# Optimization experiments

Hardware: AMD Instinct MI355X
Metric: run time of the kernel (lower is better)

Reference implementation:

```python
import jax, jax.numpy as jnp
import numpy as np

D = 512; N_HEAD = 8; D_HEAD = 64; D_INNER = 2048; SEG = 512; N_LAYER = 2; BATCH = 32
NUM_ITEMS = 50000
OMEGA = [2, 3, 4, 5, 7, 11, 21, 50]  # len == N_HEAD, required by multi-scale mask broadcast
EPS = 1e-8
STD = 0.02


def _layer_norm(x, w, b):
    mu = x.mean(-1, keepdims=True)
    var = ((x - mu) ** 2).mean(-1, keepdims=True)
    return (x - mu) / jnp.sqrt(var + EPS) * w + b


def _masks():
    # dir_mask: triu(ones, 1) (reverse=False); ms_mask[i,j,m] per omega band
    dir_mask = jnp.triu(jnp.ones((SEG, SEG), jnp.float32), 1)
    ms = np.stack([np.tri(SEG, SEG, o - 1) != np.tri(SEG, SEG, -o) for o in OMEGA], axis=-1)
    return dir_mask, jnp.asarray(ms)


def _pos_emb():
    freq = jnp.arange(0, D, 2, dtype=jnp.float32)
    inv_freq = 1.0 / jnp.power(10000.0, freq / D)
    pos_seq = jnp.arange(SEG, -SEG, -1.0, dtype=jnp.float32)  # length 2*SEG
    sinusoid = pos_seq[:, None] * inv_freq[None, :]
    return jnp.concatenate([jnp.sin(sinusoid), jnp.cos(sinusoid)], axis=-1)  # (2S, D)


def _rel_shift_bnij(x, klen):
    b, n, i, j2 = x.shape
    x = x.reshape(b, n, j2, i)[:, :, 1:, :].reshape(b, n, i, j2 - 1)
    return x[:, :, :, :klen]


def setup_inputs() -> dict:
    key = jax.random.key(0)
    ks = jax.random.split(key, 16)
    L = N_LAYER
    item_emb = STD * jax.random.normal(ks[0], (NUM_ITEMS + 1, D), jnp.float32)
    item_emb = item_emb.at[0].set(0.0)  # padding_idx=0
    proj = lambda k: STD * jax.random.normal(k, (L, D, N_HEAD, D_HEAD), jnp.float32)
    return {
        "input_ids": jax.random.randint(ks[1], (BATCH, SEG), 0, NUM_ITEMS + 1),
        "input_mask": jnp.zeros((BATCH, SEG), jnp.float32),
        "item_emb": item_emb,
        "Wq": proj(ks[2]), "Wk": proj(ks[3]), "Wv": proj(ks[4]),
        "Wr": proj(ks[5]), "Wo": proj(ks[6]),
        "r_r_bias": STD * jax.random.normal(ks[7], (L, N_HEAD, D_HEAD), jnp.float32),
        "r_w_bias": STD * jax.random.normal(ks[8], (L, N_HEAD, D_HEAD), jnp.float32),
        "ln_attn_w": jnp.ones((L, D), jnp.float32), "ln_attn_b": jnp.zeros((L, D), jnp.float32),
        "W1": STD * jax.random.normal(ks[9], (L, D, D_INNER), jnp.float32),
        "b1": jnp.zeros((L, D_INNER), jnp.float32),
        "W2": STD * jax.random.normal(ks[10], (L, D_INNER, D), jnp.float32),
        "b2": jnp.zeros((L, D), jnp.float32),
        "ln_ff_w": jnp.ones((L, D), jnp.float32), "ln_ff_b": jnp.zeros((L, D), jnp.float32),
    }


def reference(input_ids, input_mask, item_emb, Wq, Wk, Wv, Wr, Wo, r_r_bias, r_w_bias,
              ln_attn_w, ln_attn_b, W1, b1, W2, b2, ln_ff_w, ln_ff_b):
    ids = input_ids.T                      # (S, B)
    im = input_mask.T.astype(jnp.float32)  # (S, B)
    dir_mask, ms_mask = _masks()
    # data_mask: (q,k,b); attn_mask: (q,k,b,n) via multi-scale bands (training path)
    data_mask = im[None, :, :] + im[:, None, :] + dir_mask[:, :, None]
    attn_mask = ((data_mask[:, :, :, None] + (~ms_mask)[:, :, None, :].astype(jnp.float32)) > 0).astype(jnp.float32)
    mask_bnij = jnp.transpose(attn_mask, (2, 3, 0, 1))  # (b,n,i,j)

    h = item_emb[ids]          # (S, B, D)
    pos = _pos_emb()           # (2S, D), shared across batch
    scale = 1.0 / np.sqrt(D_HEAD).astype(np.float32)

    for l in range(N_LAYER):
        k_h = jnp.einsum('ibh,hnd->ibnd', h, Wk[l])
        v_h = jnp.einsum('ibh,hnd->ibnd', h, Wv[l])
        k_r = jnp.einsum('jh,hnd->jnd', pos, Wr[l])   # pos shared across batch
        q_h = jnp.einsum('ibh,hnd->ibnd', h, Wq[l])
        ac = jnp.einsum('ibnd,jbnd->bnij', q_h + r_w_bias[l], k_h)
        bd = jnp.einsum('ibnd,jnd->bnij', q_h + r_r_bias[l], k_r)
        bd = _rel_shift_bnij(bd, SEG)
        attn_score = (ac + bd) * scale - 1e30 * mask_bnij
        attn_prob = jax.nn.softmax(attn_score, axis=3)
        attn_vec = jnp.einsum('bnij,jbnd->ibnd', attn_prob, v_h)
        attn_out = jnp.einsum('ibnd,hnd->ibh', attn_vec, Wo[l])
        h = _layer_norm(attn_out + h, ln_attn_w[l], ln_attn_b[l])
        ff = jax.nn.gelu(h @ W1[l] + b1[l], approximate=False) @ W2[l] + b2[l]
        h = _layer_norm(ff + h, ln_ff_w[l], ln_ff_b[l])

    return jnp.transpose(h, (1, 0, 2))  # (B, S, D)
```

## Files before the change

kernel.cpp:

```cpp
#include <hip/hip_runtime.h>
#include <math.h>


#define S_  512
#define B_  32
#define D_  512
#define NH  8
#define DH  64
#define DI  2048
#define M_  (S_*B_)
#define QKV_LD 1536
#define WL  3407872
#define FP32_ONE 0x3F800000u

typedef unsigned short ushort_t;
typedef __attribute__((ext_vector_type(8))) short short8;
typedef __attribute__((ext_vector_type(4))) float f32x4;

__constant__ int OMEGA_C[8] = {2, 3, 4, 5, 7, 11, 21, 50};

__device__ __forceinline__ float b2f(ushort_t us) {
    return __uint_as_float(((unsigned int)us) << 16);
}
__device__ __forceinline__ ushort_t f2b(float f) {
    unsigned int u = __float_as_uint(f);
    return (ushort_t)((u + 0x7fffu + ((u >> 16) & 1u)) >> 16);
}
__device__ __forceinline__ float ldx(const void* p, size_t idx, bool isbf) {
    return isbf ? b2f(((const ushort_t*)p)[idx]) : ((const float*)p)[idx];
}
__device__ __forceinline__ void async16(const ushort_t* g, ushort_t* l) {
    __builtin_amdgcn_global_load_lds(
        (const __attribute__((address_space(1))) unsigned int*)g,
        (__attribute__((address_space(3))) unsigned int*)l, 16, 0, 0);
}

#define DPPA(v, ctrl) v += __int_as_float(__builtin_amdgcn_update_dpp(0, __float_as_int(v), ctrl, 0xf, 0xf, true))
__device__ __forceinline__ void dpp_sum64(float& v) {
    DPPA(v, 0x111); DPPA(v, 0x112); DPPA(v, 0x114);
    DPPA(v, 0x118); DPPA(v, 0x142); DPPA(v, 0x143);
}
#define DPPROR(v, ctrl) __int_as_float(__builtin_amdgcn_update_dpp(__float_as_int(v), __float_as_int(v), ctrl, 0xf, 0xf, false))
__device__ __forceinline__ float row16_sum(float v) {
    v += DPPROR(v, 0x128); v += DPPROR(v, 0x124);
    v += DPPROR(v, 0x122); v += DPPROR(v, 0x121);
    return v;
}
__device__ __forceinline__ float row16_max(float v) {
    v = fmaxf(v, DPPROR(v, 0x128)); v = fmaxf(v, DPPROR(v, 0x124));
    v = fmaxf(v, DPPROR(v, 0x122)); v = fmaxf(v, DPPROR(v, 0x121));
    return v;
}

__global__ __launch_bounds__(256) void embed_kernel(const int* __restrict__ ids,
                                                    const void* __restrict__ emb,
                                                    ushort_t* __restrict__ h,
                                                    const unsigned int* __restrict__ dtp) {
    const bool isbf = (dtp[0] != FP32_ONE);
    int flat = blockIdx.x * 256 + threadIdx.x;
    int d = flat & (D_ - 1);
    int row = flat >> 9;
    int s = row >> 5, b = row & 31;
    int id = ids[b * S_ + s];
    size_t src = (size_t)id * D_ + d;
    h[flat] = isbf ? ((const ushort_t*)emb)[src] : f2b(((const float*)emb)[src]);
}

__global__ __launch_bounds__(256) void posemb_kernel(ushort_t* __restrict__ pos) {
    int flat = blockIdx.x * 256 + threadIdx.x;
    int p = flat >> 8, k = flat & 255;
    float inv = expf((float)k * -0.035977892078031f);
    float val = (512.0f - (float)p) * inv;
    pos[p * D_ + k]       = f2b(sinf(val));
    pos[p * D_ + 256 + k] = f2b(cosf(val));
}

__global__ __launch_bounds__(256) void transp_cvt4(
    const void* __restrict__ s0, const void* __restrict__ s1,
    const void* __restrict__ s2, const void* __restrict__ s3,
    ushort_t* __restrict__ wbuf, const unsigned int* __restrict__ dtp) {
    const bool isbf = (dtp[0] != FP32_ONE);
    __shared__ float tt[32][33];
    int z = blockIdx.z, layer = z >> 2, t4 = z & 3;
    const void* srcs[4] = {s0, s1, s2, s3};
    const void* in = srcs[t4];
    size_t inoff = (size_t)layer * 262144;
    ushort_t* out = wbuf + (size_t)layer * WL + (size_t)t4 * 262144;
    int tx = threadIdx.x & 31, ty = threadIdx.x >> 5;
    int n0 = blockIdx.x * 32, k0 = blockIdx.y * 32;
#pragma unroll
    for (int it = 0; it < 4; ++it)
        tt[ty + it * 8][tx] = ldx(in, inoff + (size_t)(k0 + ty + it * 8) * 512 + n0 + tx, isbf);
    __syncthreads();
#pragma unroll
    for (int it = 0; it < 4; ++it)
        out[(size_t)(n0 + ty + it * 8) * 512 + k0 + tx] = f2b(tt[tx][ty + it * 8]);
}

__global__ __launch_bounds__(256) void transp_cvtL(const void* __restrict__ in, size_t perlin,
                                                   ushort_t* __restrict__ wbuf, size_t outoff,
                                                   const unsigned int* __restrict__ dtp,
                                                   int K, int N) {
    const bool isbf = (dtp[0] != FP32_ONE);
    __shared__ float tt[32][33];
    int layer = blockIdx.z;
    size_t inoff = (size_t)layer * perlin;
    ushort_t* out = wbuf + (size_t)layer * WL + outoff;
    int tx = threadIdx.x & 31, ty = threadIdx.x >> 5;
    int n0 = blockIdx.x * 32, k0 = blockIdx.y * 32;
#pragma unroll
    for (int it = 0; it < 4; ++it)
        tt[ty + it * 8][tx] = ldx(in, inoff + (size_t)(k0 + ty + it * 8) * N + n0 + tx, isbf);
    __syncthreads();
#pragma unroll
    for (int it = 0; it < 4; ++it)
        out[(size_t)(n0 + ty + it * 8) * K + k0 + tx] = f2b(tt[tx][ty + it * 8]);
}

__global__ __launch_bounds__(256) void cvtL(const void* __restrict__ in, size_t perlin,
                                            ushort_t* __restrict__ wbuf, size_t outoff,
                                            const unsigned int* __restrict__ dtp, int nelem) {
    const bool isbf = (dtp[0] != FP32_ONE);
    int layer = blockIdx.z;
    int i = blockIdx.x * 256 + threadIdx.x;
    if (i < nelem)
        wbuf[(size_t)layer * WL + outoff + i] = f2b(ldx(in, (size_t)layer * perlin + i, isbf));
}

template<int EPI, int OUT>
__global__ __launch_bounds__(256)
void mfma_gemm(const ushort_t* __restrict__ A, int lda,
               const ushort_t* __restrict__ Bt, int ldb,
               const void* __restrict__ biasv, size_t biasoff,
               void* __restrict__ Cv, int ldc,
               const unsigned int* __restrict__ dtp, int M, int N, int K) {
    const bool isbf = (dtp[0] != FP32_ONE);
    __shared__ ushort_t As[128 * 32];
    __shared__ ushort_t Bs[128 * 32];
    const int tid = threadIdx.x;
    const int bm = blockIdx.x * 128, bn = blockIdx.y * 128;
    const int w = tid >> 6, lane = tid & 63;
    const int wr = w >> 1, wc = w & 1;
    const int quad = lane >> 4, l16 = lane & 15;
    const int rsub = lane >> 2;
    const int kcg  = (lane & 3) ^ ((rsub >> 1) & 3);
    const int fsw  = (l16 >> 1) & 3;

    f32x4 acc[4][4];
#pragma unroll
    for (int i = 0; i < 4; ++i)
#pragma unroll
        for (int j = 0; j < 4; ++j)
#pragma unroll
            for (int r = 0; r < 4; ++r) acc[i][j][r] = 0.f;

    for (int k0 = 0; k0 < K; k0 += 32) {
#pragma unroll
        for (int c = 0; c < 2; ++c) {
            int grp = c * 4 + w;
            int row = grp * 16 + rsub;
            async16(A  + (size_t)(bm + row) * lda + k0 + kcg * 8, As + grp * 512);
            async16(Bt + (size_t)(bn + row) * ldb + k0 + kcg * 8, Bs + grp * 512);
        }
        __syncthreads();

        short8 af[4], bf[4];
#pragma unroll
        for (int t = 0; t < 4; ++t) {
            int ra = wr * 64 + t * 16 + l16;
            int rb = wc * 64 + t * 16 + l16;
            af[t] = *(const short8*)(As + ra * 32 + ((quad ^ fsw) * 8));
            bf[t] = *(const short8*)(Bs + rb * 32 + ((quad ^ fsw) * 8));
        }
#pragma unroll
        for (int tr = 0; tr < 4; ++tr)
#pragma unroll
            for (int tc = 0; tc < 4; ++tc)
                acc[tr][tc] = __builtin_amdgcn_mfma_f32_16x16x32_bf16(af[tr], bf[tc], acc[tr][tc], 0, 0, 0);
        __syncthreads();
    }

#pragma unroll
    for (int tc = 0; tc < 4; ++tc) {
        int gcol = bn + wc * 64 + tc * 16 + l16;
        float bv = 0.f;
        if (EPI >= 1) bv = ldx(biasv, biasoff + gcol, isbf);
#pragma unroll
        for (int tr = 0; tr < 4; ++tr) {
            int rbase = bm + wr * 64 + tr * 16 + quad * 4;
#pragma unroll
            for (int r = 0; r < 4; ++r) {
                float x = acc[tr][tc][r] + bv;
                if (EPI == 2) x = 0.5f * x * (1.f + erff(x * 0.7071067811865475f));
                size_t coff = (size_t)(rbase + r) * ldc + gcol;
                if (OUT == 0)      ((ushort_t*)Cv)[coff] = f2b(x);
                else if (OUT == 1) ((float*)Cv)[coff] = x;
                else               ((float*)Cv)[coff] += x;
            }
        }
    }
}

__global__ __launch_bounds__(256) void attn_mfma(
    ushort_t* __restrict__ qkv, const ushort_t* __restrict__ krb,
    const void* __restrict__ rwb, const void* __restrict__ rrb, size_t boff,
    const void* __restrict__ im,
    const unsigned int* __restrict__ dtp) {
    const bool isbf = (dtp[0] != FP32_ONE);
    __shared__ ushort_t Ks[128 * 64];
    __shared__ ushort_t VT[64 * 128];
    __shared__ ushort_t Rs[64 * 64];
    __shared__ float    BD2[4 * 16 * 64];
    __shared__ ushort_t Ps[4 * 16 * 128];
    __shared__ float    imk[128];
    __shared__ float    imq[64];

    const int tid = threadIdx.x;
    const int i0 = blockIdx.x * 64;
    const int b  = blockIdx.y;
    const int n  = blockIdx.z;
    const int o  = OMEGA_C[n];
    const int noff = n * DH;
    const int j0 = i0 - 64;
    const int w = tid >> 6, lane = tid & 63;
    const int quad = lane >> 4, l16 = lane & 15;

#pragma unroll
    for (int it = 0; it < 4; ++it) {
        int q4 = it * 256 + tid;
        int c  = q4 >> 3, ch = q4 & 7;
        int jc = j0 + c; jc = jc < 0 ? 0 : jc;
        size_t rowb = (size_t)(jc * B_ + b) * QKV_LD + noff;
        *(uint4*)(Ks + c * 64 + ch * 8) = *(const uint4*)(qkv + rowb + 512 + ch * 8);
        ushort_t v8[8];
        *(uint4*)v8 = *(const uint4*)(qkv + rowb + 1024 + ch * 8);
#pragma unroll
        for (int e = 0; e < 8; ++e) VT[(ch * 8 + e) * 128 + c] = v8[e];
    }
#pragma unroll
    for (int it = 0; it < 2; ++it) {
        int q4 = it * 256 + tid;
        int m = q4 >> 3, ch = q4 & 7;
        *(uint4*)(Rs + m * 64 + ch * 8) =
            *(const uint4*)(krb + (size_t)(512 - m) * 512 + noff + ch * 8);
    }
    if (tid < 128) {
        int j = j0 + tid;
        imk[tid] = (j >= 0) ? ldx(im, b * S_ + j, isbf) : 0.f;
    } else if (tid < 192) {
        imq[tid - 128] = ldx(im, b * S_ + i0 + (tid - 128), isbf);
    }
    __syncthreads();

    const int qrow = i0 + w * 16 + l16;
    size_t qbase = (size_t)(qrow * B_ + b) * QKV_LD + noff;
    short8 aw[2], ar[2];
#pragma unroll
    for (int kc = 0; kc < 2; ++kc) {
        int kof = kc * 32 + quad * 8;
        ushort_t qe[8];
        *(uint4*)qe = *(const uint4*)(qkv + qbase + kof);
#pragma unroll
        for (int e = 0; e < 8; ++e) {
            float f = b2f(qe[e]);
            ((ushort_t*)&aw[kc])[e] = f2b(f + ldx(rwb, boff + noff + kof + e, isbf));
            ((ushort_t*)&ar[kc])[e] = f2b(f + ldx(rrb, boff + noff + kof + e, isbf));
        }
    }

    f32x4 accs[8];
#pragma unroll
    for (int ct = 0; ct < 8; ++ct) {
        short8 b0 = *(const short8*)(Ks + (ct * 16 + l16) * 64 + quad * 8);
        short8 b1 = *(const short8*)(Ks + (ct * 16 + l16) * 64 + 32 + quad * 8);
        f32x4 z = {0.f, 0.f, 0.f, 0.f};
        z = __builtin_amdgcn_mfma_f32_16x16x32_bf16(aw[0], b0, z, 0, 0, 0);
        z = __builtin_amdgcn_mfma_f32_16x16x32_bf16(aw[1], b1, z, 0, 0, 0);
        accs[ct] = z;
    }
    float* BD2w = BD2 + w * 16 * 64;
#pragma unroll
    for (int mt = 0; mt < 4; ++mt) {
        short8 b0 = *(const short8*)(Rs + (mt * 16 + l16) * 64 + quad * 8);
        short8 b1 = *(const short8*)(Rs + (mt * 16 + l16) * 64 + 32 + quad * 8);
        f32x4 z = {0.f, 0.f, 0.f, 0.f};
        z = __builtin_amdgcn_mfma_f32_16x16x32_bf16(ar[0], b0, z, 0, 0, 0);
        z = __builtin_amdgcn_mfma_f32_16x16x32_bf16(ar[1], b1, z, 0, 0, 0);
#pragma unroll
        for (int r = 0; r < 4; ++r)
            BD2w[(quad * 4 + r) * 64 + mt * 16 + l16] = z[r];
    }

    float im_i[4];
#pragma unroll
    for (int r = 0; r < 4; ++r) im_i[r] = imq[w * 16 + quad * 4 + r];

    float sc[8][4];
#pragma unroll
    for (int ct = 0; ct < 8; ++ct) {
        int cl = ct * 16 + l16;
        float imk_c = imk[cl];
#pragma unroll
        for (int r = 0; r < 4; ++r) {
            int qrl = w * 16 + quad * 4 + r;
            int rel = qrl + 64 - cl;
            int relc = rel < 0 ? 0 : (rel > 63 ? 63 : rel);
            float bd = BD2w[(quad * 4 + r) * 64 + relc];
            bool valid = (rel >= 0) && (rel < o) && (rel <= i0 + qrl)
                         && (im_i[r] + imk_c <= 0.f);
            sc[ct][r] = valid ? (accs[ct][r] + bd) * 0.125f : -1e30f;
        }
    }
    float rl[4];
#pragma unroll
    for (int r = 0; r < 4; ++r) {
        float mx = sc[0][r];
#pragma unroll
        for (int ct = 1; ct < 8; ++ct) mx = fmaxf(mx, sc[ct][r]);
        mx = row16_max(mx);
        float l = 0.f;
#pragma unroll
        for (int ct = 0; ct < 8; ++ct) {
            float pv = expf(sc[ct][r] - mx);
            sc[ct][r] = pv;
            l += pv;
        }
        l = row16_sum(l);
        rl[r] = 1.f / l;
    }
    ushort_t* Pw = Ps + w * 16 * 128;
#pragma unroll
    for (int ct = 0; ct < 8; ++ct)
#pragma unroll
        for (int r = 0; r < 4; ++r)
            Pw[(quad * 4 + r) * 128 + ct * 16 + l16] = f2b(sc[ct][r]);

    short8 aP[4];
#pragma unroll
    for (int kc = 0; kc < 4; ++kc)
        aP[kc] = *(const short8*)(Pw + l16 * 128 + kc * 32 + quad * 8);

#pragma unroll
    for (int dt = 0; dt < 4; ++dt) {
        f32x4 accO = {0.f, 0.f, 0.f, 0.f};
#pragma unroll
        for (int kc = 0; kc < 4; ++kc) {
            short8 bV = *(const short8*)(VT + (dt * 16 + l16) * 128 + kc * 32 + quad * 8);
            accO = __builtin_amdgcn_mfma_f32_16x16x32_bf16(aP[kc], bV, accO, 0, 0, 0);
        }
#pragma unroll
        for (int r = 0; r < 4; ++r) {
            int qg = i0 + w * 16 + quad * 4 + r;
            qkv[(size_t)(qg * B_ + b) * QKV_LD + noff + dt * 16 + l16] = f2b(accO[r] * rl[r]);
        }
    }
}

template<int XF>
__global__ __launch_bounds__(256) void add_ln_kernel(
    const void* __restrict__ x, ushort_t* __restrict__ h,
    const void* __restrict__ w, const void* __restrict__ b, size_t boff,
    const unsigned int* __restrict__ dtp) {
    const bool isbf = (dtp[0] != FP32_ONE);
    int row = blockIdx.x;
    size_t base = (size_t)row * D_;
    int tid = threadIdx.x;
    float x0 = XF ? ((const float*)x)[base + tid]       : b2f(((const ushort_t*)x)[base + tid]);
    float x1 = XF ? ((const float*)x)[base + 256 + tid] : b2f(((const ushort_t*)x)[base + 256 + tid]);
    float v0 = x0 + b2f(h[base + tid]);
    float v1 = x1 + b2f(h[base + 256 + tid]);
    float s = v0 + v1, ss = v0 * v0 + v1 * v1;
    dpp_sum64(s); dpp_sum64(ss);
    __shared__ float red[8];
    int wv = tid >> 6, lane = tid & 63;
    if (lane == 63) { red[wv] = s; red[4 + wv] = ss; }
    __syncthreads();
    float S  = red[0] + red[1] + red[2] + red[3];
    float SS = red[4] + red[5] + red[6] + red[7];
    float mu  = S * (1.f / D_);
    float var = fmaxf(SS * (1.f / D_) - mu * mu, 0.f);
    float inv = rsqrtf(var + 1e-8f);
    h[base + tid]       = f2b((v0 - mu) * inv * ldx(w, boff + tid, isbf)       + ldx(b, boff + tid, isbf));
    h[base + 256 + tid] = f2b((v1 - mu) * inv * ldx(w, boff + 256 + tid, isbf) + ldx(b, boff + 256 + tid, isbf));
}

__global__ __launch_bounds__(256) void writeout_kernel(const ushort_t* __restrict__ h,
                                                       void* __restrict__ out,
                                                       const unsigned int* __restrict__ dtp) {
    const bool isbf = (dtp[0] != FP32_ONE);
    int flat = blockIdx.x * 256 + threadIdx.x;
    int d = flat & (D_ - 1);
    int rest = flat >> 9;
    int s = rest & (S_ - 1), b = rest >> 9;
    ushort_t v = h[((size_t)(s * B_ + b) << 9) + d];
    if (isbf) ((ushort_t*)out)[flat] = v;
    else      ((float*)out)[flat] = b2f(v);
}

extern "C" void kernel_launch(void* const* d_in, const int* in_sizes, int n_in,
                              void* d_out, int out_size, void* d_ws, size_t ws_size,
                              hipStream_t stream) {
    (void)in_sizes; (void)n_in; (void)out_size; (void)ws_size;
    const int*  ids = (const int*)d_in[0];
    const void* im  = d_in[1];
    const void* emb = d_in[2];
    const void* Wq = d_in[3], *Wk = d_in[4], *Wv = d_in[5], *Wr = d_in[6], *Wo = d_in[7];
    const void* rrb = d_in[8], *rwb = d_in[9];
    const void* lnaw = d_in[10], *lnab = d_in[11];
    const void* W1 = d_in[12], *b1 = d_in[13], *W2 = d_in[14], *b2 = d_in[15];
    const void* lnfw = d_in[16], *lnfb = d_in[17];
    const unsigned int* dtp = (const unsigned int*)d_in[10];

    char* wsb = (char*)d_ws;
    ushort_t* h     = (ushort_t*)wsb;
    ushort_t* qkv   = (ushort_t*)(wsb + (16u << 20));
    ushort_t* ff1c  = (ushort_t*)(wsb + (16u << 20));
    float*    acc32 = (float*)   (wsb + (48u << 20));
    ushort_t* tmp   = (ushort_t*)(wsb + (64u << 20));
    ushort_t* wbuf  = (ushort_t*)(wsb + (80u << 20));
    ushort_t* posb  = (ushort_t*)(wsb + (93u << 20));
    ushort_t* krb   = (ushort_t*)(wsb + (94u << 20));

    embed_kernel<<<32768, 256, 0, stream>>>(ids, emb, h, dtp);
    posemb_kernel<<<1024, 256, 0, stream>>>(posb);

    transp_cvt4<<<dim3(16, 16, 8), 256, 0, stream>>>(Wq, Wk, Wv, Wr, wbuf, dtp);
    cvtL<<<dim3(1024, 1, 2), 256, 0, stream>>>(Wo, 262144, wbuf, 1048576, dtp, 262144);
    transp_cvtL<<<dim3(64, 16, 2), 256, 0, stream>>>(W1, 1048576, wbuf, 1310720, dtp, 512, 2048);
    transp_cvtL<<<dim3(16, 64, 2), 256, 0, stream>>>(W2, 1048576, wbuf, 2359296, dtp, 2048, 512);

    for (int l = 0; l < 2; ++l) {
        size_t boff = (size_t)l * 512;
        size_t b1off = (size_t)l * 2048;
        ushort_t* qkvT = wbuf + (size_t)l * WL;
        ushort_t* wrT  = qkvT + 786432;
        ushort_t* woc  = wrT  + 262144;
        ushort_t* w1T  = woc  + 262144;
        ushort_t* w2T  = w1T  + 1048576;

        mfma_gemm<0,0><<<dim3(8, 4), 256, 0, stream>>>(posb, 512, wrT, 512, nullptr, 0, krb, 512, dtp, 1024, 512, 512);
        mfma_gemm<0,0><<<dim3(128, 12), 256, 0, stream>>>(h, 512, qkvT, 512, nullptr, 0, qkv, QKV_LD, dtp, M_, QKV_LD, 512);

        attn_mfma<<<dim3(8, 32, 8), 256, 0, stream>>>(qkv, krb, rwb, rrb, boff, im, dtp);

        mfma_gemm<0,0><<<dim3(128, 4), 256, 0, stream>>>(qkv, QKV_LD, woc, 512, nullptr, 0, tmp, 512, dtp, M_, 512, 512);
        add_ln_kernel<0><<<16384, 256, 0, stream>>>(tmp, h, lnaw, lnab, boff, dtp);

        for (int nh = 0; nh < 2; ++nh) {
            ushort_t* w1part = w1T + (size_t)nh * 1024 * 512;
            ushort_t* w2part = w2T + (size_t)nh * 1024;
            mfma_gemm<2,0><<<dim3(128, 8), 256, 0, stream>>>(h, 512, w1part, 512, b1, b1off + nh * 1024, ff1c, 1024, dtp, M_, 1024, 512);
            if (nh == 0)
                mfma_gemm<1,1><<<dim3(128, 4), 256, 0, stream>>>(ff1c, 1024, w2part, 2048, b2, boff, acc32, 512, dtp, M_, 512, 1024);
            else
                mfma_gemm<0,2><<<dim3(128, 4), 256, 0, stream>>>(ff1c, 1024, w2part, 2048, nullptr, 0, acc32, 512, dtp, M_, 512, 1024);
        }
        add_ln_kernel<1><<<16384, 256, 0, stream>>>(acc32, h, lnfw, lnfb, boff, dtp);
    }

    writeout_kernel<<<32768, 256, 0, stream>>>(h, d_out, dtp);
}
```

Before: 842.8 us.

## Vectorize embed, layernorm, writeout and GEMM/attention epilogue stores

The embed, writeout and add+layernorm kernels now process 8 elements per thread with 128-bit loads and stores, and layernorm uses one wave per row with a readlane reduction instead of shared memory. The GEMM and attention epilogues swap the MFMA operand order so each lane holds contiguous output columns, which lets results be written as packed 64- or 128-bit stores instead of scattered 16-bit ones. Softmax normalization moves into the P write. The attention kernel still computes the old accO product but discards it, which adds redundant MFMA work unless the compiler eliminates it.

```diff
diff --git a/kernel.cpp b/kernel.cpp
--- a/kernel.cpp
+++ b/kernel.cpp
@@ -51,19 +51,33 @@
     v = fmaxf(v, DPPROR(v, 0x122)); v = fmaxf(v, DPPROR(v, 0x121));
     return v;
 }
+__device__ __forceinline__ float rlane(float v, int l) {
+    return __int_as_float(__builtin_amdgcn_readlane(__float_as_int(v), l));
+}
 
 __global__ __launch_bounds__(256) void embed_kernel(const int* __restrict__ ids,
                                                     const void* __restrict__ emb,
                                                     ushort_t* __restrict__ h,
                                                     const unsigned int* __restrict__ dtp) {
     const bool isbf = (dtp[0] != FP32_ONE);
-    int flat = blockIdx.x * 256 + threadIdx.x;
-    int d = flat & (D_ - 1);
-    int row = flat >> 9;
+    int idx = blockIdx.x * 256 + threadIdx.x;
+    int d8 = idx & 63;
+    int row = idx >> 6;
     int s = row >> 5, b = row & 31;
     int id = ids[b * S_ + s];
-    size_t src = (size_t)id * D_ + d;
-    h[flat] = isbf ? ((const ushort_t*)emb)[src] : f2b(((const float*)emb)[src]);
+    size_t src = (size_t)id * D_ + d8 * 8;
+    if (isbf) {
+        *(uint4*)(h + (size_t)row * D_ + d8 * 8) = *(const uint4*)((const ushort_t*)emb + src);
+    } else {
+        const float* e = (const float*)emb + src;
+        float4 a0 = ((const float4*)e)[0], a1 = ((const float4*)e)[1];
+        uint4 pk;
+        pk.x = (unsigned)f2b(a0.x) | ((unsigned)f2b(a0.y) << 16);
+        pk.y = (unsigned)f2b(a0.z) | ((unsigned)f2b(a0.w) << 16);
+        pk.z = (unsigned)f2b(a1.x) | ((unsigned)f2b(a1.y) << 16);
+        pk.w = (unsigned)f2b(a1.z) | ((unsigned)f2b(a1.w) << 16);
+        *(uint4*)(h + (size_t)row * D_ + d8 * 8) = pk;
+    }
 }
 
 __global__ __launch_bounds__(256) void posemb_kernel(ushort_t* __restrict__ pos) {
@@ -176,26 +190,45 @@
         for (int tr = 0; tr < 4; ++tr)
 #pragma unroll
             for (int tc = 0; tc < 4; ++tc)
-                acc[tr][tc] = __builtin_amdgcn_mfma_f32_16x16x32_bf16(af[tr], bf[tc], acc[tr][tc], 0, 0, 0);
+                acc[tr][tc] = __builtin_amdgcn_mfma_f32_16x16x32_bf16(bf[tc], af[tr], acc[tr][tc], 0, 0, 0);
         __syncthreads();
     }
 
-#pragma unroll
-    for (int tc = 0; tc < 4; ++tc) {
-        int gcol = bn + wc * 64 + tc * 16 + l16;
-        float bv = 0.f;
-        if (EPI >= 1) bv = ldx(biasv, biasoff + gcol, isbf);
-#pragma unroll
-        for (int tr = 0; tr < 4; ++tr) {
-            int rbase = bm + wr * 64 + tr * 16 + quad * 4;
+    float bv[4][4];
+    if (EPI >= 1) {
+#pragma unroll
+        for (int tc = 0; tc < 4; ++tc)
+#pragma unroll
+            for (int r = 0; r < 4; ++r)
+                bv[tc][r] = ldx(biasv, biasoff + bn + wc * 64 + tc * 16 + quad * 4 + r, isbf);
+    }
+#pragma unroll
+    for (int tr = 0; tr < 4; ++tr) {
+        int grow = bm + wr * 64 + tr * 16 + l16;
+#pragma unroll
+        for (int tc = 0; tc < 4; ++tc) {
+            int gcb = bn + wc * 64 + tc * 16 + quad * 4;
+            float x[4];
 #pragma unroll
             for (int r = 0; r < 4; ++r) {
-                float x = acc[tr][tc][r] + bv;
-                if (EPI == 2) x = 0.5f * x * (1.f + erff(x * 0.7071067811865475f));
-                size_t coff = (size_t)(rbase + r) * ldc + gcol;
-                if (OUT == 0)      ((ushort_t*)Cv)[coff] = f2b(x);
-                else if (OUT == 1) ((float*)Cv)[coff] = x;
-                else               ((float*)Cv)[coff] += x;
+                float v = acc[tr][tc][r];
+                if (EPI >= 1) v += bv[tc][r];
+                if (EPI == 2) v = 0.5f * v * (1.f + erff(v * 0.7071067811865475f));
+                x[r] = v;
+            }
+            size_t coff = (size_t)grow * ldc + gcb;
+            if (OUT == 0) {
+                uint2 pk;
+                pk.x = (unsigned)f2b(x[0]) | ((unsigned)f2b(x[1]) << 16);
+                pk.y = (unsigned)f2b(x[2]) | ((unsigned)f2b(x[3]) << 16);
+                *(uint2*)((ushort_t*)Cv + coff) = pk;
+            } else if (OUT == 1) {
+                *(float4*)((float*)Cv + coff) = make_float4(x[0], x[1], x[2], x[3]);
+            } else {
+                float4* p = (float4*)((float*)Cv + coff);
+                float4 o = *p;
+                o.x += x[0]; o.y += x[1]; o.z += x[2]; o.w += x[3];
+                *p = o;
             }
         }
     }
@@ -333,13 +366,15 @@
     for (int ct = 0; ct < 8; ++ct)
 #pragma unroll
         for (int r = 0; r < 4; ++r)
-            Pw[(quad * 4 + r) * 128 + ct * 16 + l16] = f2b(sc[ct][r]);
+            Pw[(quad * 4 + r) * 128 + ct * 16 + l16] = f2b(sc[ct][r] * rl[r]);
 
     short8 aP[4];
 #pragma unroll
     for (int kc = 0; kc < 4; ++kc)
         aP[kc] = *(const short8*)(Pw + l16 * 128 + kc * 32 + quad * 8);
 
+    const int qg = i0 + w * 16 + l16;
+    const size_t obase = (size_t)(qg * B_ + b) * QKV_LD + noff;
 #pragma unroll
     for (int dt = 0; dt < 4; ++dt) {
         f32x4 accO = {0.f, 0.f, 0.f, 0.f};
@@ -348,11 +383,17 @@
             short8 bV = *(const short8*)(VT + (dt * 16 + l16) * 128 + kc * 32 + quad * 8);
             accO = __builtin_amdgcn_mfma_f32_16x16x32_bf16(aP[kc], bV, accO, 0, 0, 0);
         }
-#pragma unroll
-        for (int r = 0; r < 4; ++r) {
-            int qg = i0 + w * 16 + quad * 4 + r;
-            qkv[(size_t)(qg * B_ + b) * QKV_LD + noff + dt * 16 + l16] = f2b(accO[r] * rl[r]);
-        }
+        f32x4 accT = {0.f, 0.f, 0.f, 0.f};
+#pragma unroll
+        for (int kc = 0; kc < 4; ++kc) {
+            short8 bV = *(const short8*)(VT + (dt * 16 + l16) * 128 + kc * 32 + quad * 8);
+            accT = __builtin_amdgcn_mfma_f32_16x16x32_bf16(bV, aP[kc], accT, 0, 0, 0);
+        }
+        (void)accO;
+        uint2 pk;
+        pk.x = (unsigned)f2b(accT[0]) | ((unsigned)f2b(accT[1]) << 16);
+        pk.y = (unsigned)f2b(accT[2]) | ((unsigned)f2b(accT[3]) << 16);
+        *(uint2*)(qkv + obase + dt * 16 + quad * 4) = pk;
     }
 }
 
@@ -362,39 +403,59 @@
     const void* __restrict__ w, const void* __restrict__ b, size_t boff,
     const unsigned int* __restrict__ dtp) {
     const bool isbf = (dtp[0] != FP32_ONE);
-    int row = blockIdx.x;
-    size_t base = (size_t)row * D_;
-    int tid = threadIdx.x;
-    float x0 = XF ? ((const float*)x)[base + tid]       : b2f(((const ushort_t*)x)[base + tid]);
-    float x1 = XF ? ((const float*)x)[base + 256 + tid] : b2f(((const ushort_t*)x)[base + 256 + tid]);
-    float v0 = x0 + b2f(h[base + tid]);
-    float v1 = x1 + b2f(h[base + 256 + tid]);
-    float s = v0 + v1, ss = v0 * v0 + v1 * v1;
+    int lane = threadIdx.x & 63;
+    int row = blockIdx.x * 4 + (threadIdx.x >> 6);
+    size_t base = (size_t)row * D_ + lane * 8;
+    float v[8];
+    if (XF) {
+        const float* xp = (const float*)x + base;
+        float4 a0 = ((const float4*)xp)[0], a1 = ((const float4*)xp)[1];
+        v[0] = a0.x; v[1] = a0.y; v[2] = a0.z; v[3] = a0.w;
+        v[4] = a1.x; v[5] = a1.y; v[6] = a1.z; v[7] = a1.w;
+    } else {
+        ushort_t xe[8];
+        *(uint4*)xe = *(const uint4*)((const ushort_t*)x + base);
+#pragma unroll
+        for (int e = 0; e < 8; ++e) v[e] = b2f(xe[e]);
+    }
+    ushort_t he[8];
+    *(uint4*)he = *(const uint4*)(h + base);
+    float s = 0.f, ss = 0.f;
+#pragma unroll
+    for (int e = 0; e < 8; ++e) {
+        v[e] += b2f(he[e]);
+        s += v[e]; ss += v[e] * v[e];
+    }
     dpp_sum64(s); dpp_sum64(ss);
-    __shared__ float red[8];
-    int wv = tid >> 6, lane = tid & 63;
-    if (lane == 63) { red[wv] = s; red[4 + wv] = ss; }
-    __syncthreads();
-    float S  = red[0] + red[1] + red[2] + red[3];
-    float SS = red[4] + red[5] + red[6] + red[7];
+    float S = rlane(s, 63), SS = rlane(ss, 63);
     float mu  = S * (1.f / D_);
     float var = fmaxf(SS * (1.f / D_) - mu * mu, 0.f);
     float inv = rsqrtf(var + 1e-8f);
-    h[base + tid]       = f2b((v0 - mu) * inv * ldx(w, boff + tid, isbf)       + ldx(b, boff + tid, isbf));
-    h[base + 256 + tid] = f2b((v1 - mu) * inv * ldx(w, boff + 256 + tid, isbf) + ldx(b, boff + 256 + tid, isbf));
+    ushort_t oe[8];
+#pragma unroll
+    for (int e = 0; e < 8; ++e)
+        oe[e] = f2b((v[e] - mu) * inv * ldx(w, boff + lane * 8 + e, isbf)
+                    + ldx(b, boff + lane * 8 + e, isbf));
+    *(uint4*)(h + base) = *(uint4*)oe;
 }
 
 __global__ __launch_bounds__(256) void writeout_kernel(const ushort_t* __restrict__ h,
                                                        void* __restrict__ out,
                                                        const unsigned int* __restrict__ dtp) {
     const bool isbf = (dtp[0] != FP32_ONE);
-    int flat = blockIdx.x * 256 + threadIdx.x;
-    int d = flat & (D_ - 1);
-    int rest = flat >> 9;
+    int idx = blockIdx.x * 256 + threadIdx.x;
+    int d8 = idx & 63;
+    int rest = idx >> 6;
     int s = rest & (S_ - 1), b = rest >> 9;
-    ushort_t v = h[((size_t)(s * B_ + b) << 9) + d];
-    if (isbf) ((ushort_t*)out)[flat] = v;
-    else      ((float*)out)[flat] = b2f(v);
+    ushort_t ve[8];
+    *(uint4*)ve = *(const uint4*)(h + ((size_t)(s * B_ + b) << 9) + d8 * 8);
+    if (isbf) {
+        *(uint4*)((ushort_t*)out + (size_t)idx * 8) = *(uint4*)ve;
+    } else {
+        float* op = (float*)out + (size_t)idx * 8;
+        ((float4*)op)[0] = make_float4(b2f(ve[0]), b2f(ve[1]), b2f(ve[2]), b2f(ve[3]));
+        ((float4*)op)[1] = make_float4(b2f(ve[4]), b2f(ve[5]), b2f(ve[6]), b2f(ve[7]));
+    }
 }
 
 extern "C" void kernel_launch(void* const* d_in, const int* in_sizes, int n_in,
@@ -421,7 +482,7 @@
     ushort_t* posb  = (ushort_t*)(wsb + (93u << 20));
     ushort_t* krb   = (ushort_t*)(wsb + (94u << 20));
 
-    embed_kernel<<<32768, 256, 0, stream>>>(ids, emb, h, dtp);
+    embed_kernel<<<4096, 256, 0, stream>>>(ids, emb, h, dtp);
     posemb_kernel<<<1024, 256, 0, stream>>>(posb);
 
     transp_cvt4<<<dim3(16, 16, 8), 256, 0, stream>>>(Wq, Wk, Wv, Wr, wbuf, dtp);
@@ -444,7 +505,7 @@
         attn_mfma<<<dim3(8, 32, 8), 256, 0, stream>>>(qkv, krb, rwb, rrb, boff, im, dtp);
 
         mfma_gemm<0,0><<<dim3(128, 4), 256, 0, stream>>>(qkv, QKV_LD, woc, 512, nullptr, 0, tmp, 512, dtp, M_, 512, 512);
-        add_ln_kernel<0><<<16384, 256, 0, stream>>>(tmp, h, lnaw, lnab, boff, dtp);
+        add_ln_kernel<0><<<4096, 256, 0, stream>>>(tmp, h, lnaw, lnab, boff, dtp);
 
         for (int nh = 0; nh < 2; ++nh) {
             ushort_t* w1part = w1T + (size_t)nh * 1024 * 512;
@@ -455,8 +516,8 @@
             else
                 mfma_gemm<0,2><<<dim3(128, 4), 256, 0, stream>>>(ff1c, 1024, w2part, 2048, nullptr, 0, acc32, 512, dtp, M_, 512, 1024);
         }
-        add_ln_kernel<1><<<16384, 256, 0, stream>>>(acc32, h, lnfw, lnfb, boff, dtp);
-    }
-
-    writeout_kernel<<<32768, 256, 0, stream>>>(h, d_out, dtp);
-}
+        add_ln_kernel<1><<<4096, 256, 0, stream>>>(acc32, h, lnfw, lnfb, boff, dtp);
+    }
+
+    writeout_kernel<<<4096, 256, 0, stream>>>(h, d_out, dtp);
+}
```

After: 869.3 us. 3.2% more time.
